# Kernel tuning notes

Hardware: AMD Instinct MI355X
Metric: run time of the kernel (lower is better)

The kernel has to match this reference:

```python
import jax, jax.numpy as jnp
import numpy as np

N = 1_000_000      # occupied input voxels
NREF = 400_000     # occupied reference (target) voxels on the stride-2 grid
CIN = 32
COUT = 64
G = 256            # input spatial grid extent per axis
B = 4              # batch size (ME batch index in coords[:, 0])
PRIME = 2654435761 # odd -> bijective multiplier mod 2^26


def _decode_np(ids, g):
    z = ids % g; ids = ids // g
    y = ids % g; ids = ids // g
    x = ids % g; b = ids // g
    return np.stack([b, x, y, z], axis=1).astype(np.int32)


def setup_inputs() -> dict:
    key = jax.random.key(0)
    k1, k2, k3 = jax.random.split(key, 3)
    # unique input voxel coordinates on a B x G^3 grid (bijection mod 2^26)
    ids_in = (np.arange(N, dtype=np.int64) * PRIME) % (B * G ** 3)
    coords = _decode_np(ids_in, G)                      # [N,4] (b,x,y,z), unique
    # unique reference coordinates on the stride-2 output grid
    gh = G // 2
    ids_ref = (np.arange(NREF, dtype=np.int64) * PRIME) % (B * gh ** 3)
    ref = _decode_np(ids_ref, gh)
    ref[:, 1:] *= 2                                     # ME tensor-stride-2 coords
    feats = jax.random.normal(k1, (N, CIN), jnp.float32)
    W = jax.random.normal(k2, (8, CIN, COUT), jnp.float32) * (1.0 / np.sqrt(8 * CIN))
    b = jax.random.normal(k3, (COUT,), jnp.float32) * 0.01
    return {"feats": feats, "W": W, "b": b,
            "coords": jnp.asarray(coords), "ref_coords": jnp.asarray(ref)}


def _ravel(c, step):
    # faithful to get_target_by_sp_tensor: batch-major ravel of 4 columns
    return c[:, 3] + c[:, 2] * step + c[:, 1] * step * step + c[:, 0] * step * step * step


def reference(feats, W, b, coords, ref_coords):
    n = coords.shape[0]
    # --- hash table of input voxels (sorted keys + permuted features) ---
    in_key = ((coords[:, 0] * G + coords[:, 1]) * G + coords[:, 2]) * G + coords[:, 3]
    order = jnp.argsort(in_key)
    skeys = in_key[order]
    sfeats = feats[order]
    # --- output coordinates: stride-2 downsample (kernel=2, stride=2) ---
    p = coords.at[:, 1:].set((coords[:, 1:] // 2) * 2)
    pkey = ((p[:, 0] * G + p[:, 1]) * G + p[:, 2]) * G + p[:, 3]
    out_key = jnp.unique(pkey, size=n, fill_value=-1)   # sorted, padded with -1
    valid = out_key >= 0
    ok = jnp.where(valid, out_key, 0)
    oz = ok % G; r = ok // G
    oy = r % G; r = r // G
    ox = r % G; ob = r // G
    out_coords = jnp.where(valid[:, None], jnp.stack([ob, ox, oy, oz], axis=1), -1)
    # --- sparse conv: gather the 2x2x2 children of each output voxel ---
    acc = jnp.zeros((n, W.shape[2]), feats.dtype)
    offsets = [(dx, dy, dz) for dx in (0, 1) for dy in (0, 1) for dz in (0, 1)]
    for i, (dx, dy, dz) in enumerate(offsets):
        ckey = out_key + dx * G * G + dy * G + dz
        idx = jnp.clip(jnp.searchsorted(skeys, ckey), 0, n - 1)
        found = (skeys[idx] == ckey) & valid
        f = jnp.where(found[:, None], sfeats[idx], 0.0)
        acc = acc + f @ W[i]
    out_feats = jnp.where(valid[:, None], acc + b, 0.0)
    # --- pruning mask: ravel + isin, faithful to get_target_by_sp_tensor ---
    step = jnp.maximum(out_coords.max(), ref_coords.max()).astype(jnp.int32) + 1
    min_value = jnp.minimum(out_coords.min(), ref_coords.min())
    shift = jnp.where(min_value < 0, -min_value, 0)
    oc = out_coords.at[:, 1:].add(shift)
    rc = ref_coords.at[:, 1:].add(shift)
    out1d = _ravel(oc, step)
    ref1d = _ravel(rc, step)
    sref = jnp.sort(ref1d)
    j = jnp.clip(jnp.searchsorted(sref, out1d), 0, sref.shape[0] - 1)
    mask = (sref[j] == out1d) & valid
    out_feats = jnp.where(mask[:, None], out_feats, 0.0)
    return out_coords, out_feats, mask
```

## Files before the change

### kernel.cpp

```cpp
#include <hip/hip_runtime.h>

#define WORDS_P  (1u << 18)
#define NBLK2    1024

typedef float f4_native __attribute__((ext_vector_type(4)));

__device__ __forceinline__ unsigned k23_of(int b, int x, int y, int z) {
  return ((unsigned)b << 21) | ((unsigned)(x >> 1) << 14) |
         ((unsigned)(y >> 1) << 7) | (unsigned)(z >> 1);
}

__global__ __launch_bounds__(256) void fill_ws(f4_native* __restrict__ wsz, size_t n4) {
  size_t stride = (size_t)gridDim.x * 256u;
  f4_native z = {0.f, 0.f, 0.f, 0.f};
  for (size_t i = (size_t)blockIdx.x * 256u + threadIdx.x; i < n4; i += stride)
    wsz[i] = z;
}

__global__ __launch_bounds__(256) void build_fill(const int4* __restrict__ coords, int n,
                                                  const int4* __restrict__ ref, int nref,
                                                  unsigned* __restrict__ parbm,
                                                  unsigned* __restrict__ refbm,
                                                  f4_native* __restrict__ ofm,
                                                  size_t n4_ofm) {
  unsigned tid = blockIdx.x * 256u + threadIdx.x;
  unsigned nthr = gridDim.x * 256u;
  for (unsigned i = tid; i < (unsigned)(n + nref); i += nthr) {
    if (i < (unsigned)n) {
      int4 c = coords[i];
      unsigned k = k23_of(c.x, c.y, c.z, c.w);
      atomicOr(&parbm[k >> 5], 1u << (k & 31));
    } else {
      int4 c = ref[i - (unsigned)n];
      unsigned k = k23_of(c.x, c.y, c.z, c.w);
      atomicOr(&refbm[k >> 5], 1u << (k & 31));
    }
  }
  f4_native z = {0.f, 0.f, 0.f, 0.f};
  for (size_t i = tid; i < n4_ofm; i += nthr)
    __builtin_nontemporal_store(z, &ofm[i]);
}

__global__ __launch_bounds__(256) void pop2(const unsigned* __restrict__ parbm,
                                            unsigned* __restrict__ refbm,
                                            unsigned* __restrict__ bsums) {
  __shared__ unsigned s[256];
  unsigned t = threadIdx.x;
  unsigned w = blockIdx.x * 256u + t;
  unsigned p = parbm[w];
  unsigned m = p & refbm[w];
  refbm[w] = m;
  s[t] = __popc(p); __syncthreads();
  for (int off = 128; off > 0; off >>= 1) { if (t < (unsigned)off) s[t] += s[t + off]; __syncthreads(); }
  if (t == 0) bsums[blockIdx.x] = s[0];
  __syncthreads();
  s[t] = __popc(m); __syncthreads();
  for (int off = 128; off > 0; off >>= 1) { if (t < (unsigned)off) s[t] += s[t + off]; __syncthreads(); }
  if (t == 0) bsums[NBLK2 + blockIdx.x] = s[0];
}

__global__ __launch_bounds__(256) void prefix2b(const unsigned* __restrict__ parbm,
                                                const unsigned* __restrict__ maskbm,
                                                const unsigned* __restrict__ bsums,
                                                unsigned* __restrict__ parpre,
                                                unsigned* __restrict__ maskpre,
                                                unsigned* __restrict__ clist,
                                                unsigned* __restrict__ counter) {
  __shared__ unsigned s[256];
  __shared__ unsigned basP_s, basM_s;
  unsigned t = threadIdx.x, blk = blockIdx.x;
  unsigned accP = 0, accM = 0;
  for (unsigned idx = t; idx < blk; idx += 256u) {
    accP += bsums[idx];
    accM += bsums[NBLK2 + idx];
  }
  s[t] = accP; __syncthreads();
  for (int off = 128; off > 0; off >>= 1) { if (t < (unsigned)off) s[t] += s[t + off]; __syncthreads(); }
  if (t == 0) basP_s = s[0];
  __syncthreads();
  s[t] = accM; __syncthreads();
  for (int off = 128; off > 0; off >>= 1) { if (t < (unsigned)off) s[t] += s[t + off]; __syncthreads(); }
  if (t == 0) basM_s = s[0];
  __syncthreads();
  unsigned basP = basP_s, basM = basM_s;

  unsigned w = blk * 256u + t;
  unsigned pw = parbm[w], mw = maskbm[w];
  unsigned cp = __popc(pw), cm = __popc(mw);
  s[t] = cp; __syncthreads();
  for (int off = 1; off < 256; off <<= 1) {
    unsigned v = (t >= (unsigned)off) ? s[t - off] : 0u;
    __syncthreads(); s[t] += v; __syncthreads();
  }
  unsigned ppre = basP + ((t == 0) ? 0u : s[t - 1]);
  parpre[w] = ppre;
  unsigned plast = basP + s[255];
  __syncthreads();
  s[t] = cm; __syncthreads();
  for (int off = 1; off < 256; off <<= 1) {
    unsigned v = (t >= (unsigned)off) ? s[t - off] : 0u;
    __syncthreads(); s[t] += v; __syncthreads();
  }
  unsigned mpre = basM + ((t == 0) ? 0u : s[t - 1]);
  maskpre[w] = mpre;
  for (unsigned k = 0; k < cm * 8u; k++) clist[mpre * 8u + k] = 0u;
  if (blk == NBLK2 - 1u && t == 255u) {
    counter[0] = basM + s[255];
    counter[1] = plast;
  }
}

__global__ __launch_bounds__(256) void scatter_emit(const int4* __restrict__ coords, int n,
                                                    const unsigned* __restrict__ parbm,
                                                    const unsigned* __restrict__ parpre,
                                                    const unsigned* __restrict__ maskbm,
                                                    const unsigned* __restrict__ maskpre,
                                                    const unsigned* __restrict__ counter,
                                                    unsigned* __restrict__ clist,
                                                    unsigned* __restrict__ mrow,
                                                    float4* __restrict__ out_coords,
                                                    float* __restrict__ out_mask,
                                                    int nbN) {
  if ((int)blockIdx.x < nbN) {
    int i = blockIdx.x * 256 + threadIdx.x;
    if (i >= n) return;
    int4 c = coords[i];
    unsigned k = k23_of(c.x, c.y, c.z, c.w);
    unsigned w = k >> 5, b = k & 31u;
    unsigned mw = maskbm[w];
    if ((mw >> b) & 1u) {
      unsigned j = maskpre[w] + __popc(mw & ((1u << b) - 1u));
      unsigned off = (((unsigned)c.y & 1u) << 2) | (((unsigned)c.z & 1u) << 1) |
                     ((unsigned)c.w & 1u);
      clist[j * 8u + off] = (unsigned)i + 1u;
    }
    return;
  }
  if ((int)blockIdx.x < nbN + (int)NBLK2) {
    unsigned w = (blockIdx.x - nbN) * 256u + threadIdx.x;
    unsigned bits = parbm[w];
    if (!bits) return;
    unsigned mb = maskbm[w];
    unsigned r = parpre[w];
    unsigned j = maskpre[w];
    while (bits) {
      unsigned b = (unsigned)__ffs((int)bits) - 1u;
      bits &= bits - 1u;
      unsigned k = (w << 5) | b;
      float bb = (float)(k >> 21);
      float x = (float)(((k >> 14) & 127u) << 1);
      float y = (float)(((k >> 7) & 127u) << 1);
      float z = (float)((k & 127u) << 1);
      out_coords[r] = make_float4(bb, x, y, z);
      if ((mb >> b) & 1u) {
        out_mask[r] = 1.0f;
        mrow[j++] = r;
      }
      r++;
    }
    return;
  }
  unsigned P = counter[1];
  unsigned idx = (blockIdx.x - nbN - NBLK2) * 256u + threadIdx.x;
  unsigned ntail = (unsigned)n - P;
  float4 m1 = make_float4(-1.f, -1.f, -1.f, -1.f);
  for (unsigned i = idx; i < ntail; i += 64u * 256u) out_coords[P + i] = m1;
}

__global__ __launch_bounds__(1024, 8) void conv_lds(const float* __restrict__ feats,
                                                    const float* __restrict__ Wg,
                                                    const float* __restrict__ bias,
                                                    const unsigned* __restrict__ clist,
                                                    const unsigned* __restrict__ mrow,
                                                    const unsigned* __restrict__ counter,
                                                    float* __restrict__ out_feats) {
  __shared__ float lw[16384];
  for (unsigned t = threadIdx.x; t < 4096u; t += 1024u)
    ((float4*)lw)[t] = ((const float4*)Wg)[t];
  __syncthreads();

  unsigned lane = threadIdx.x & 63u;
  unsigned wave = blockIdx.x * 16u + (threadIdx.x >> 6);
  unsigned nwaves = gridDim.x * 16u;
  unsigned M = counter[0];
  float bv = bias[lane];
  for (unsigned j = wave; j < M; j += nwaves) {
    unsigned r = mrow[j];
    uint4 c0 = *(const uint4*)(clist + (size_t)j * 8u);
    uint4 c1 = *(const uint4*)(clist + (size_t)j * 8u + 4u);
    unsigned cs[8] = {c0.x, c0.y, c0.z, c0.w, c1.x, c1.y, c1.z, c1.w};
    float acc = bv;
#pragma unroll
    for (int i = 0; i < 8; i++) {
      unsigned v = (unsigned)__builtin_amdgcn_readfirstlane((int)cs[i]);
      if (v) {
        const float* f = feats + (size_t)(v - 1u) * 32u;
        const float* wl = lw + i * 2048 + lane;
#pragma unroll
        for (int k = 0; k < 32; k++) acc = fmaf(f[k], wl[k * 64], acc);
      }
    }
    out_feats[(size_t)r * 64u + lane] = acc;
  }
}

extern "C" void kernel_launch(void* const* d_in, const int* in_sizes, int n_in,
                              void* d_out, int out_size, void* d_ws, size_t ws_size,
                              hipStream_t stream) {
  const float* feats = (const float*)d_in[0];
  const float* W     = (const float*)d_in[1];
  const float* bias  = (const float*)d_in[2];
  const int4*  coords = (const int4*)d_in[3];
  const int4*  ref    = (const int4*)d_in[4];
  int N    = in_sizes[0] / 32;
  int NREF = in_sizes[4] / 4;

  float* out_coords = (float*)d_out;
  float* out_feats  = out_coords + (size_t)N * 4;
  float* out_mask   = out_feats + (size_t)N * 64;

  char* ws = (char*)d_ws;
  unsigned* parbm   = (unsigned*)(ws);
  unsigned* refbm   = (unsigned*)(ws + (1u << 20));
  unsigned* maskbm  = refbm;
  unsigned* clist   = (unsigned*)(ws + (2u << 20));
  unsigned* parpre  = (unsigned*)(ws + (15u << 20));
  unsigned* maskpre = (unsigned*)(ws + (16u << 20));
  unsigned* mrow    = (unsigned*)(ws + (17u << 20));
  unsigned* bsums   = (unsigned*)(ws + (19u << 20));
  unsigned* counter = (unsigned*)(ws + (19u << 20) + 16384);

  int nbN = (N + 255) / 256;

  fill_ws<<<64, 256, 0, stream>>>((f4_native*)ws, (size_t)(2u << 20) / 16u);
  build_fill<<<2048, 256, 0, stream>>>(coords, N, ref, NREF, parbm, refbm,
                                       (f4_native*)out_feats,
                                       (size_t)N * 65u * 4u / 16u);
  pop2<<<NBLK2, 256, 0, stream>>>(parbm, refbm, bsums);
  prefix2b<<<NBLK2, 256, 0, stream>>>(parbm, maskbm, bsums, parpre, maskpre, clist,
                                      counter);
  scatter_emit<<<nbN + NBLK2 + 64, 256, 0, stream>>>(coords, N, parbm, parpre, maskbm,
                                                     maskpre, counter, clist, mrow,
                                                     (float4*)out_coords, out_mask, nbN);
  conv_lds<<<512, 1024, 0, stream>>>(feats, W, bias, clist, mrow, counter, out_feats);
}
```

Before: 130.5 us.

## Fuse scan into single-pass decoupled lookback and skip zeroing masked feature rows

Merges the popcount, prefix and coordinate-emit kernels into one scan_emit kernel that uses a decoupled-lookback prefix over 64-bit flag/aggregate words, which removes two launches and the parpre round trip. The zero-fill of out_feats moves from build_fill into the conv kernel. That fill now skips rows the conv will write, using a new rowinfo array, and out_mask and tail entries are written explicitly. The cost is a serialized spin on lookback flags by thread 0 of each block, plus an extra rowinfo read per float4 in the fill loop.

Measured after the change: 161.8 us. +24.0%, slower.

```diff
diff --git a/kernel.cpp b/kernel.cpp
--- a/kernel.cpp
+++ b/kernel.cpp
@@ -17,12 +17,10 @@
     wsz[i] = z;
 }
 
-__global__ __launch_bounds__(256) void build_fill(const int4* __restrict__ coords, int n,
-                                                  const int4* __restrict__ ref, int nref,
-                                                  unsigned* __restrict__ parbm,
-                                                  unsigned* __restrict__ refbm,
-                                                  f4_native* __restrict__ ofm,
-                                                  size_t n4_ofm) {
+__global__ __launch_bounds__(256) void build_bm(const int4* __restrict__ coords, int n,
+                                                const int4* __restrict__ ref, int nref,
+                                                unsigned* __restrict__ parbm,
+                                                unsigned* __restrict__ refbm) {
   unsigned tid = blockIdx.x * 256u + threadIdx.x;
   unsigned nthr = gridDim.x * 256u;
   for (unsigned i = tid; i < (unsigned)(n + nref); i += nthr) {
@@ -36,65 +34,69 @@
       atomicOr(&refbm[k >> 5], 1u << (k & 31));
     }
   }
-  f4_native z = {0.f, 0.f, 0.f, 0.f};
-  for (size_t i = tid; i < n4_ofm; i += nthr)
-    __builtin_nontemporal_store(z, &ofm[i]);
-}
-
-__global__ __launch_bounds__(256) void pop2(const unsigned* __restrict__ parbm,
-                                            unsigned* __restrict__ refbm,
-                                            unsigned* __restrict__ bsums) {
+}
+
+__global__ __launch_bounds__(256) void scan_emit(const unsigned* __restrict__ parbm,
+                                                 unsigned* __restrict__ refbm,
+                                                 unsigned long long* __restrict__ look,
+                                                 unsigned* __restrict__ counter,
+                                                 unsigned* __restrict__ maskpre,
+                                                 unsigned* __restrict__ clist,
+                                                 unsigned* __restrict__ mrow,
+                                                 unsigned* __restrict__ rowinfo,
+                                                 float4* __restrict__ out_coords,
+                                                 float* __restrict__ out_mask) {
   __shared__ unsigned s[256];
-  unsigned t = threadIdx.x;
-  unsigned w = blockIdx.x * 256u + t;
-  unsigned p = parbm[w];
-  unsigned m = p & refbm[w];
-  refbm[w] = m;
-  s[t] = __popc(p); __syncthreads();
+  __shared__ unsigned aggP_s, aggM_s, basP_s, basM_s;
+  unsigned t = threadIdx.x, blk = blockIdx.x;
+  unsigned w = blk * 256u + t;
+  unsigned pw = parbm[w];
+  unsigned mw = pw & refbm[w];
+  refbm[w] = mw;
+  unsigned cp = __popc(pw), cm = __popc(mw);
+
+  s[t] = cp; __syncthreads();
   for (int off = 128; off > 0; off >>= 1) { if (t < (unsigned)off) s[t] += s[t + off]; __syncthreads(); }
-  if (t == 0) bsums[blockIdx.x] = s[0];
-  __syncthreads();
-  s[t] = __popc(m); __syncthreads();
+  if (t == 0) aggP_s = s[0];
+  __syncthreads();
+  s[t] = cm; __syncthreads();
   for (int off = 128; off > 0; off >>= 1) { if (t < (unsigned)off) s[t] += s[t + off]; __syncthreads(); }
-  if (t == 0) bsums[NBLK2 + blockIdx.x] = s[0];
-}
-
-__global__ __launch_bounds__(256) void prefix2b(const unsigned* __restrict__ parbm,
-                                                const unsigned* __restrict__ maskbm,
-                                                const unsigned* __restrict__ bsums,
-                                                unsigned* __restrict__ parpre,
-                                                unsigned* __restrict__ maskpre,
-                                                unsigned* __restrict__ clist,
-                                                unsigned* __restrict__ counter) {
-  __shared__ unsigned s[256];
-  __shared__ unsigned basP_s, basM_s;
-  unsigned t = threadIdx.x, blk = blockIdx.x;
-  unsigned accP = 0, accM = 0;
-  for (unsigned idx = t; idx < blk; idx += 256u) {
-    accP += bsums[idx];
-    accM += bsums[NBLK2 + idx];
-  }
-  s[t] = accP; __syncthreads();
-  for (int off = 128; off > 0; off >>= 1) { if (t < (unsigned)off) s[t] += s[t + off]; __syncthreads(); }
-  if (t == 0) basP_s = s[0];
-  __syncthreads();
-  s[t] = accM; __syncthreads();
-  for (int off = 128; off > 0; off >>= 1) { if (t < (unsigned)off) s[t] += s[t + off]; __syncthreads(); }
-  if (t == 0) basM_s = s[0];
+  if (t == 0) aggM_s = s[0];
+  __syncthreads();
+
+  if (t == 0) {
+    unsigned aggP = aggP_s, aggM = aggM_s;
+    unsigned long long va = (1ULL << 62) | ((unsigned long long)aggP << 25) |
+                            (unsigned long long)aggM;
+    atomicExch(&look[blk], va);
+    unsigned basP = 0, basM = 0;
+    int p = (int)blk - 1;
+    while (p >= 0) {
+      unsigned long long u;
+      do { u = atomicAdd(&look[p], 0ULL); } while ((u >> 62) == 0ULL);
+      basP += (unsigned)((u >> 25) & 0x1FFFFFFu);
+      basM += (unsigned)(u & 0x1FFFFFFu);
+      if ((u >> 62) == 2ULL) break;
+      p--;
+    }
+    unsigned long long vi = (2ULL << 62) |
+        ((unsigned long long)(basP + aggP) << 25) | (unsigned long long)(basM + aggM);
+    atomicExch(&look[blk], vi);
+    basP_s = basP; basM_s = basM;
+    if (blk == NBLK2 - 1u) {
+      counter[0] = basM + aggM;
+      counter[1] = basP + aggP;
+    }
+  }
   __syncthreads();
   unsigned basP = basP_s, basM = basM_s;
 
-  unsigned w = blk * 256u + t;
-  unsigned pw = parbm[w], mw = maskbm[w];
-  unsigned cp = __popc(pw), cm = __popc(mw);
   s[t] = cp; __syncthreads();
   for (int off = 1; off < 256; off <<= 1) {
     unsigned v = (t >= (unsigned)off) ? s[t - off] : 0u;
     __syncthreads(); s[t] += v; __syncthreads();
   }
   unsigned ppre = basP + ((t == 0) ? 0u : s[t - 1]);
-  parpre[w] = ppre;
-  unsigned plast = basP + s[255];
   __syncthreads();
   s[t] = cm; __syncthreads();
   for (int off = 1; off < 256; off <<= 1) {
@@ -104,20 +106,31 @@
   unsigned mpre = basM + ((t == 0) ? 0u : s[t - 1]);
   maskpre[w] = mpre;
   for (unsigned k = 0; k < cm * 8u; k++) clist[mpre * 8u + k] = 0u;
-  if (blk == NBLK2 - 1u && t == 255u) {
-    counter[0] = basM + s[255];
-    counter[1] = plast;
-  }
-}
-
-__global__ __launch_bounds__(256) void scatter_emit(const int4* __restrict__ coords, int n,
-                                                    const unsigned* __restrict__ parbm,
-                                                    const unsigned* __restrict__ parpre,
+
+  unsigned r = ppre, j = mpre, bits = pw;
+  while (bits) {
+    unsigned b = (unsigned)__ffs((int)bits) - 1u;
+    bits &= bits - 1u;
+    unsigned k = (w << 5) | b;
+    float bb = (float)(k >> 21);
+    float x = (float)(((k >> 14) & 127u) << 1);
+    float y = (float)(((k >> 7) & 127u) << 1);
+    float z = (float)((k & 127u) << 1);
+    out_coords[r] = make_float4(bb, x, y, z);
+    bool masked = (mw >> b) & 1u;
+    out_mask[r] = masked ? 1.0f : 0.0f;
+    if (masked) { mrow[j] = r; rowinfo[r] = j + 1u; j++; }
+    else rowinfo[r] = 0u;
+    r++;
+  }
+}
+
+__global__ __launch_bounds__(256) void scatter_tail(const int4* __restrict__ coords, int n,
                                                     const unsigned* __restrict__ maskbm,
                                                     const unsigned* __restrict__ maskpre,
                                                     const unsigned* __restrict__ counter,
                                                     unsigned* __restrict__ clist,
-                                                    unsigned* __restrict__ mrow,
+                                                    unsigned* __restrict__ rowinfo,
                                                     float4* __restrict__ out_coords,
                                                     float* __restrict__ out_mask,
                                                     int nbN) {
@@ -136,48 +149,43 @@
     }
     return;
   }
-  if ((int)blockIdx.x < nbN + (int)NBLK2) {
-    unsigned w = (blockIdx.x - nbN) * 256u + threadIdx.x;
-    unsigned bits = parbm[w];
-    if (!bits) return;
-    unsigned mb = maskbm[w];
-    unsigned r = parpre[w];
-    unsigned j = maskpre[w];
-    while (bits) {
-      unsigned b = (unsigned)__ffs((int)bits) - 1u;
-      bits &= bits - 1u;
-      unsigned k = (w << 5) | b;
-      float bb = (float)(k >> 21);
-      float x = (float)(((k >> 14) & 127u) << 1);
-      float y = (float)(((k >> 7) & 127u) << 1);
-      float z = (float)((k & 127u) << 1);
-      out_coords[r] = make_float4(bb, x, y, z);
-      if ((mb >> b) & 1u) {
-        out_mask[r] = 1.0f;
-        mrow[j++] = r;
-      }
-      r++;
-    }
-    return;
-  }
   unsigned P = counter[1];
-  unsigned idx = (blockIdx.x - nbN - NBLK2) * 256u + threadIdx.x;
+  unsigned idx = (blockIdx.x - nbN) * 256u + threadIdx.x;
   unsigned ntail = (unsigned)n - P;
   float4 m1 = make_float4(-1.f, -1.f, -1.f, -1.f);
-  for (unsigned i = idx; i < ntail; i += 64u * 256u) out_coords[P + i] = m1;
-}
-
-__global__ __launch_bounds__(1024, 8) void conv_lds(const float* __restrict__ feats,
-                                                    const float* __restrict__ Wg,
-                                                    const float* __restrict__ bias,
-                                                    const unsigned* __restrict__ clist,
-                                                    const unsigned* __restrict__ mrow,
-                                                    const unsigned* __restrict__ counter,
-                                                    float* __restrict__ out_feats) {
+  for (unsigned i = idx; i < ntail; i += 64u * 256u) {
+    out_coords[P + i] = m1;
+    out_mask[P + i] = 0.0f;
+    rowinfo[P + i] = 0u;
+  }
+}
+
+__global__ __launch_bounds__(1024, 8) void conv_fill(const float* __restrict__ feats,
+                                                     const float* __restrict__ Wg,
+                                                     const float* __restrict__ bias,
+                                                     const unsigned* __restrict__ clist,
+                                                     const unsigned* __restrict__ mrow,
+                                                     const unsigned* __restrict__ rowinfo,
+                                                     const unsigned* __restrict__ counter,
+                                                     int n,
+                                                     float* __restrict__ out_feats) {
   __shared__ float lw[16384];
   for (unsigned t = threadIdx.x; t < 4096u; t += 1024u)
     ((float4*)lw)[t] = ((const float4*)Wg)[t];
   __syncthreads();
+
+  unsigned tid = blockIdx.x * 1024u + threadIdx.x;
+  unsigned nthr = gridDim.x * 1024u;
+
+  {
+    f4_native z = {0.f, 0.f, 0.f, 0.f};
+    size_t n4 = (size_t)n * 16u;
+    f4_native* of = (f4_native*)out_feats;
+    for (size_t i = tid; i < n4; i += nthr) {
+      unsigned row = (unsigned)(i >> 4);
+      if (rowinfo[row] == 0u) __builtin_nontemporal_store(z, &of[i]);
+    }
+  }
 
   unsigned lane = threadIdx.x & 63u;
   unsigned wave = blockIdx.x * 16u + (threadIdx.x >> 6);
@@ -222,25 +230,23 @@
   char* ws = (char*)d_ws;
   unsigned* parbm   = (unsigned*)(ws);
   unsigned* refbm   = (unsigned*)(ws + (1u << 20));
-  unsigned* maskbm  = refbm;
-  unsigned* clist   = (unsigned*)(ws + (2u << 20));
-  unsigned* parpre  = (unsigned*)(ws + (15u << 20));
+  unsigned long long* look = (unsigned long long*)(ws + (2u << 20));
+  unsigned* counter = (unsigned*)(ws + (2u << 20) + 8192);
+  unsigned* clist   = (unsigned*)(ws + (3u << 20));
   unsigned* maskpre = (unsigned*)(ws + (16u << 20));
   unsigned* mrow    = (unsigned*)(ws + (17u << 20));
-  unsigned* bsums   = (unsigned*)(ws + (19u << 20));
-  unsigned* counter = (unsigned*)(ws + (19u << 20) + 16384);
+  unsigned* rowinfo = (unsigned*)(ws + (19u << 20));
 
   int nbN = (N + 255) / 256;
 
-  fill_ws<<<64, 256, 0, stream>>>((f4_native*)ws, (size_t)(2u << 20) / 16u);
-  build_fill<<<2048, 256, 0, stream>>>(coords, N, ref, NREF, parbm, refbm,
-                                       (f4_native*)out_feats,
-                                       (size_t)N * 65u * 4u / 16u);
-  pop2<<<NBLK2, 256, 0, stream>>>(parbm, refbm, bsums);
-  prefix2b<<<NBLK2, 256, 0, stream>>>(parbm, maskbm, bsums, parpre, maskpre, clist,
-                                      counter);
-  scatter_emit<<<nbN + NBLK2 + 64, 256, 0, stream>>>(coords, N, parbm, parpre, maskbm,
-                                                     maskpre, counter, clist, mrow,
-                                                     (float4*)out_coords, out_mask, nbN);
-  conv_lds<<<512, 1024, 0, stream>>>(feats, W, bias, clist, mrow, counter, out_feats);
-}
+  fill_ws<<<128, 256, 0, stream>>>((f4_native*)ws,
+                                   ((size_t)(2u << 20) + 16384u) / 16u);
+  build_bm<<<2048, 256, 0, stream>>>(coords, N, ref, NREF, parbm, refbm);
+  scan_emit<<<NBLK2, 256, 0, stream>>>(parbm, refbm, look, counter, maskpre, clist,
+                                       mrow, rowinfo, (float4*)out_coords, out_mask);
+  scatter_tail<<<nbN + 64, 256, 0, stream>>>(coords, N, refbm, maskpre, counter,
+                                             clist, rowinfo, (float4*)out_coords,
+                                             out_mask, nbN);
+  conv_fill<<<512, 1024, 0, stream>>>(feats, W, bias, clist, mrow, rowinfo, counter,
+                                      N, out_feats);
+}
```
